# Optimization experiments

Hardware: AMD Instinct MI355X
Metric: run time of the kernel (lower is better)

## Reference

```python
import jax, jax.numpy as jnp
import numpy as np

B, N, D, E, H = 8, 2048, 256, 16, 8
CAP = max(min(N, int(N * 2.0 / E)), 4)  # eval capacity_factor = 2.0 -> 256
EPS = 1e-9
LOSS_COEF = 0.01


def _excl_cumsum(t, axis):
    return jnp.cumsum(t, axis=axis) - t


def _top2_gating(x, w_gating):
    # x: (B, N, D); w_gating: (D, E)
    raw = jax.nn.softmax(jnp.einsum('bnd,de->bne', x, w_gating), axis=-1)
    idx1 = jnp.argmax(raw, axis=-1)
    g1 = jnp.max(raw, axis=-1)
    m1 = jax.nn.one_hot(idx1, E, dtype=raw.dtype)
    gates2 = raw * (1.0 - m1)
    idx2 = jnp.argmax(gates2, axis=-1)
    g2 = jnp.max(gates2, axis=-1)
    m2 = jax.nn.one_hot(idx2, E, dtype=raw.dtype)
    denom = g1 + g2 + EPS
    g1 = g1 / denom
    g2 = g2 / denom
    # load-balance loss
    density_1 = m1.mean(axis=-2)          # (B, E)
    proxy = raw.mean(axis=-2)             # (B, E)
    loss = (proxy * density_1).mean() * float(E * E)
    # second policy == 'all': keep mask_2 as-is
    pos1 = _excl_cumsum(m1, -2) * m1
    m1 = m1 * (pos1 < float(CAP)).astype(m1.dtype)
    m1_count = m1.sum(axis=-2, keepdims=True)
    m1_flat = m1.sum(axis=-1)             # (B, N)
    pos1 = pos1.sum(axis=-1)              # (B, N)
    g1 = g1 * m1_flat
    pos2 = (_excl_cumsum(m2, -2) + m1_count) * m2
    m2 = m2 * (pos2 < float(CAP)).astype(m2.dtype)
    m2_flat = m2.sum(axis=-1)
    pos2 = pos2.sum(axis=-1)
    g2 = g2 * m2_flat
    oh_e1 = jax.nn.one_hot(idx1, E, dtype=raw.dtype)
    oh_e2 = jax.nn.one_hot(idx2, E, dtype=raw.dtype)
    oh_c1 = jax.nn.one_hot(pos1.astype(jnp.int32), CAP, dtype=raw.dtype)
    oh_c2 = jax.nn.one_hot(pos2.astype(jnp.int32), CAP, dtype=raw.dtype)
    # combine: (B, N, E, CAP); note torch applies mask_flat twice (idempotent)
    combine = ((g1 * m1_flat)[..., None, None] * oh_e1[..., :, None] * oh_c1[..., None, :]
               + (g2 * m2_flat)[..., None, None] * oh_e2[..., :, None] * oh_c2[..., None, :])
    dispatch = (combine > 0).astype(combine.dtype)
    return dispatch, combine, loss


def _mixer(xe, audio, Wq, Wkv, Wp, bp):
    # CrossModalMixer, eval mode (dropouts = identity)
    # xe: (B, CAP, D); audio: (B, 1, D)
    b, n, c = xe.shape
    dh = c // H
    scale = dh ** -0.5
    q = (audio @ Wq).reshape(b, 1, H, dh).transpose(0, 2, 1, 3)   # (b,h,1,dh)
    kv = (xe @ Wkv).reshape(b, n, 2, H, dh)
    k = kv[:, :, 0].transpose(0, 2, 1, 3)                          # (b,h,n,dh)
    v = kv[:, :, 1].transpose(0, 2, 1, 3)
    attn = jax.nn.softmax(jnp.einsum('bhqd,bhkd->bhqk', q, k) * scale, axis=-1)
    o = jnp.einsum('bhqk,bhkd->bhqd', attn, v).transpose(0, 2, 1, 3).reshape(b, 1, c)
    gate = jax.nn.sigmoid(o @ Wp + bp)                             # (b,1,c)
    return xe * gate                                               # einsum('bnc,bc->bnc')


def setup_inputs():
    ks = jax.random.split(jax.random.key(0), 7)
    return {
        'x': jax.random.normal(ks[0], (B, N, D), jnp.float32),
        'audio_feat': jax.random.normal(ks[1], (B, 1, D), jnp.float32),
        'w_gating': jax.random.normal(ks[2], (D, E), jnp.float32),
        'Wq': jax.random.normal(ks[3], (E, D, D), jnp.float32) * 0.02,
        'Wkv': jax.random.normal(ks[4], (E, D, 2 * D), jnp.float32) * 0.02,
        'Wp': jax.random.normal(ks[5], (E, D, D), jnp.float32) * 0.02,
        'bp': jnp.zeros((E, D), jnp.float32),
    }


def reference(x, audio_feat, w_gating, Wq, Wkv, Wp, bp):
    dispatch, combine, loss = _top2_gating(x, w_gating)
    expert_in = jnp.einsum('bnd,bnec->ebcd', x, dispatch)          # (E, B, CAP, D)
    outs = jax.vmap(_mixer, in_axes=(0, None, 0, 0, 0, 0))(expert_in, audio_feat, Wq, Wkv, Wp, bp)
    out = jnp.einsum('ebcd,bnec->bnd', outs, combine)
    return out, loss * LOSS_COEF
```

## Files before the change

kernel.cpp:

```cpp
#include <hip/hip_runtime.h>
#include <cstdint>
#include <cstddef>

#define BB 8
#define NN 2048
#define DD 256
#define EE 16
#define HH 8
#define CAPC 256
#define BN (BB*NN)
#define EB (EE*BB)

__global__ __launch_bounds__(256) void fused_gq_kernel(
    const float* __restrict__ x, const float* __restrict__ wg,
    const float* __restrict__ audio, const float* __restrict__ Wq,
    const float* __restrict__ Wkv,
    int* __restrict__ idx1a, int* __restrict__ idx2a,
    float* __restrict__ g1a, float* __restrict__ g2a,
    float* __restrict__ raw_part, float* __restrict__ cnt_part,
    float* __restrict__ rws)
{
  __shared__ union SM {
    struct { float wgS[DD*EE]; float lgp[4][64][17]; } g;
    struct { float aS[DD][8]; float qpart[8][32][9]; float qS[32][8];
             float wkS[DD][33]; } q;
  } sm;
  int tid = threadIdx.x;

  if (blockIdx.x < 256) {
    for (int t = tid; t < DD*EE; t += 256) sm.g.wgS[t] = wg[t];
    __syncthreads();
    int tk = tid & 63, kc = tid >> 6;
    int token0 = blockIdx.x * 64;
    int token = token0 + tk;
    const float4* xr = (const float4*)(x + (size_t)token*DD + kc*64);
    const float4* wg4 = (const float4*)sm.g.wgS;
    float lg[16];
#pragma unroll
    for (int e = 0; e < 16; ++e) lg[e] = 0.f;
#pragma unroll
    for (int d4 = 0; d4 < 16; ++d4) {
      float4 xv = xr[d4];
      float xa[4] = {xv.x, xv.y, xv.z, xv.w};
#pragma unroll
      for (int dd = 0; dd < 4; ++dd) {
        int d = kc*64 + d4*4 + dd;
        float xc = xa[dd];
#pragma unroll
        for (int j = 0; j < 4; ++j) {
          float4 w = wg4[d*4 + j];
          lg[4*j+0] += xc*w.x; lg[4*j+1] += xc*w.y;
          lg[4*j+2] += xc*w.z; lg[4*j+3] += xc*w.w;
        }
      }
    }
#pragma unroll
    for (int e = 0; e < 16; ++e) sm.g.lgp[kc][tk][e] = lg[e];
    __syncthreads();
    if (tid < 64) {
      int lane = tid;
      float l[16];
#pragma unroll
      for (int e = 0; e < 16; ++e)
        l[e] = sm.g.lgp[0][lane][e] + sm.g.lgp[1][lane][e]
             + sm.g.lgp[2][lane][e] + sm.g.lgp[3][lane][e];
      float mx = l[0];
#pragma unroll
      for (int e = 1; e < 16; ++e) mx = fmaxf(mx, l[e]);
      float p[16]; float s = 0.f;
#pragma unroll
      for (int e = 0; e < 16; ++e) { p[e] = expf(l[e] - mx); s += p[e]; }
      int i1 = 0; float b1 = p[0];
#pragma unroll
      for (int e = 1; e < 16; ++e) { if (p[e] > b1) { b1 = p[e]; i1 = e; } }
      float b2 = (i1 == 0) ? 0.f : p[0]; int i2 = 0;
#pragma unroll
      for (int e = 1; e < 16; ++e) { float v = (e == i1) ? 0.f : p[e]; if (v > b2) { b2 = v; i2 = e; } }
      float inv = 1.f / s;
      float g1 = b1*inv, g2 = b2*inv;
      float den = g1 + g2 + 1e-9f;
      g1 /= den; g2 /= den;
      int tok = token0 + lane;
      idx1a[tok] = i1; idx2a[tok] = i2;
      g1a[tok] = g1;   g2a[tok] = g2;
      int blk = blockIdx.x;
#pragma unroll
      for (int e = 0; e < 16; ++e) {
        float v = p[e] * inv;
        v += __shfl_down(v, 32); v += __shfl_down(v, 16);
        v += __shfl_down(v, 8);  v += __shfl_down(v, 4);
        v += __shfl_down(v, 2);  v += __shfl_down(v, 1);
        unsigned long long mb = __ballot(i1 == e);
        if (lane == 0) {
          raw_part[blk*16 + e] = v;
          cnt_part[blk*16 + e] = (float)__popcll(mb);
        }
      }
    }
  } else {
    int eh = blockIdx.x - 256;
    int e = eh >> 3, h = eh & 7;
    for (int i = tid; i < 2048; i += 256) { int b = i >> 8, k = i & 255; sm.q.aS[k][b] = audio[b*DD + k]; }
    __syncthreads();
    int j = tid & 31, kg = tid >> 5;
    const float* wq = Wq + (size_t)e*DD*DD + h*32 + j;
    float acc[8] = {0,0,0,0,0,0,0,0};
#pragma unroll
    for (int i = 0; i < 32; ++i) {
      int k = kg*32 + i;
      float w = wq[(size_t)k*DD];
      float4 a0 = *(const float4*)&sm.q.aS[k][0];
      float4 a1 = *(const float4*)&sm.q.aS[k][4];
      acc[0]+=w*a0.x; acc[1]+=w*a0.y; acc[2]+=w*a0.z; acc[3]+=w*a0.w;
      acc[4]+=w*a1.x; acc[5]+=w*a1.y; acc[6]+=w*a1.z; acc[7]+=w*a1.w;
    }
#pragma unroll
    for (int b = 0; b < 8; ++b) sm.q.qpart[kg][j][b] = acc[b];
    const float* wkbase = Wkv + (size_t)e*(DD*2*DD) + h*32;
    float4 stg[8];
#pragma unroll
    for (int m = 0; m < 8; ++m) {
      int row = m*32 + (tid >> 3), c4 = tid & 7;
      stg[m] = *(const float4*)(wkbase + (size_t)row*(2*DD) + c4*4);
    }
#pragma unroll
    for (int m = 0; m < 8; ++m) {
      int row = m*32 + (tid >> 3), c4 = tid & 7;
      sm.q.wkS[row][c4*4+0] = stg[m].x; sm.q.wkS[row][c4*4+1] = stg[m].y;
      sm.q.wkS[row][c4*4+2] = stg[m].z; sm.q.wkS[row][c4*4+3] = stg[m].w;
    }
    __syncthreads();
    {
      int jj = tid >> 3, b = tid & 7;
      float s = 0.f;
#pragma unroll
      for (int g = 0; g < 8; ++g) s += sm.q.qpart[g][jj][b];
      sm.q.qS[jj][b] = s;
    }
    __syncthreads();
    int d = tid;
    float racc[8] = {0,0,0,0,0,0,0,0};
#pragma unroll
    for (int jj = 0; jj < 32; ++jj) {
      float w = sm.q.wkS[d][jj];
      float4 q0 = *(const float4*)&sm.q.qS[jj][0];
      float4 q1 = *(const float4*)&sm.q.qS[jj][4];
      racc[0]+=w*q0.x; racc[1]+=w*q0.y; racc[2]+=w*q0.z; racc[3]+=w*q0.w;
      racc[4]+=w*q1.x; racc[5]+=w*q1.y; racc[6]+=w*q1.z; racc[7]+=w*q1.w;
    }
#pragma unroll
    for (int b = 0; b < 8; ++b)
      rws[((size_t)(e*8 + b))*2048 + d*8 + h] = racc[b];
  }
}

__global__ __launch_bounds__(256) void scan_kernel(
    const int* __restrict__ idx1a, const int* __restrict__ idx2a,
    float* __restrict__ g1a, float* __restrict__ g2a, int* __restrict__ slot_token,
    const float* __restrict__ raw_part, const float* __restrict__ cnt_part,
    const float* __restrict__ Wkv, const float* __restrict__ Wp,
    float* __restrict__ dummy,
    float* __restrict__ out_loss)
{
  int tid = threadIdx.x;
  if (blockIdx.x >= BB) {
    int pid = (blockIdx.x - BB)*256 + tid;
    const float4* wk4 = (const float4*)Wkv;
    const float4* wp4 = (const float4*)Wp;
    float s = 0.f;
    for (int i = pid; i < 786432; i += 56*256) {
      float4 v = (i < 524288) ? wk4[i] : wp4[i - 524288];
      s += v.x + v.y + v.z + v.w;
    }
    if (s != 0.f) dummy[pid & 1023] = s;
    return;
  }
  __shared__ unsigned long long m1s[16][32], m2s[16][32];
  __shared__ int wp1[16][32], wp2[16][32], mcnt[16];
  int b = blockIdx.x;
  int wave = tid >> 6, lane = tid & 63;
  for (int i = tid; i < 16*CAPC; i += 256) {
    int e = i >> 8, s = i & 255;
    slot_token[(e*BB + b)*CAPC + s] = -1;
  }
  for (int w = wave; w < 32; w += 4) {
    int token = b*NN + w*64 + lane;
    int i1 = idx1a[token], i2 = idx2a[token];
#pragma unroll
    for (int e = 0; e < 16; ++e) {
      unsigned long long ma = __ballot(i1 == e);
      unsigned long long mb = __ballot(i2 == e);
      if (lane == 0) { m1s[e][w] = ma; m2s[e][w] = mb; }
    }
  }
  __syncthreads();
  if (tid < 16) {
    int run = 0;
    for (int w = 0; w < 32; ++w) { wp1[tid][w] = run; run += (int)__popcll(m1s[tid][w]); }
    mcnt[tid] = run < CAPC ? run : CAPC;
  } else if (tid < 32) {
    int e2 = tid - 16; int run = 0;
    for (int w = 0; w < 32; ++w) { wp2[e2][w] = run; run += (int)__popcll(m2s[e2][w]); }
  }
  __syncthreads();
  for (int w = wave; w < 32; w += 4) {
    int token = b*NN + w*64 + lane;
    int i1 = idx1a[token], i2 = idx2a[token];
    unsigned long long lt = (1ull << lane) - 1ull;
    int pos1 = wp1[i1][w] + (int)__popcll(m1s[i1][w] & lt);
    float g1 = g1a[token];
    bool k1 = pos1 < CAPC;
    g1a[token] = k1 ? g1 : 0.f;
    if (k1) slot_token[(i1*BB + b)*CAPC + pos1] = token;
    int pos2 = mcnt[i2] + wp2[i2][w] + (int)__popcll(m2s[i2][w] & lt);
    float g2 = g2a[token];
    bool k2 = pos2 < CAPC;
    g2a[token] = k2 ? g2 : 0.f;
    if (k2 && g2 > 0.f) slot_token[(i2*BB + b)*CAPC + pos2] = token;
  }
  if (blockIdx.x == 0) {
    float v = 0.f;
    if (tid < 128) {
      int bb = tid >> 4, e = tid & 15;
      float rs = 0.f, cs = 0.f;
#pragma unroll 4
      for (int k = 0; k < 32; ++k) {
        rs += raw_part[(bb*32 + k)*16 + e];
        cs += cnt_part[(bb*32 + k)*16 + e];
      }
      v = (rs * (1.f/(float)NN)) * (cs * (1.f/(float)NN));
    }
    v += __shfl_down(v, 32); v += __shfl_down(v, 16); v += __shfl_down(v, 8);
    v += __shfl_down(v, 4);  v += __shfl_down(v, 2);  v += __shfl_down(v, 1);
    __shared__ float r4[4];
    if ((tid & 63) == 0) r4[tid >> 6] = v;
    __syncthreads();
    if (tid == 0)
      out_loss[0] = (r4[0]+r4[1]+r4[2]+r4[3]) * ((float)(EE*EE) / (float)(BB*EE)) * 0.01f;
  }
}

__global__ __launch_bounds__(512) void expert_kernel(
    const float* __restrict__ x, const float* __restrict__ rws,
    const int* __restrict__ slot_token, const float* __restrict__ Wkv,
    const float* __restrict__ Wp, const float* __restrict__ bp,
    float* __restrict__ gateW)
{
  __shared__ float rS[DD][8];
  __shared__ int   tokS[CAPC];
  __shared__ float lp[2][CAPC][9];
  __shared__ float aST[CAPC][8];
  __shared__ float part[2][8][DD];
  __shared__ float xaS[8][DD];
  __shared__ float oS[DD];
  __shared__ float op[2][DD];
  int tid = threadIdx.x;
  int eb = blockIdx.x;
  int e  = eb >> 3;

  {
    const float4* rin = (const float4*)(rws + (size_t)eb*2048);
    ((float4*)rS)[tid] = rin[tid];
    if (tid < CAPC) tokS[tid] = slot_token[eb*CAPC + tid];
  }
  __syncthreads();

  {
    int s = tid >> 1, q = tid & 1;
    int token = tokS[s];
    float l[8] = {0,0,0,0,0,0,0,0};
    if (token >= 0) {
      const float4* xr = (const float4*)(x + (size_t)token*DD) + q;
#pragma unroll
      for (int i = 0; i < 32; ++i) {
        float4 xv = xr[i*2];
        float xa[4] = {xv.x, xv.y, xv.z, xv.w};
#pragma unroll
        for (int dd = 0; dd < 4; ++dd) {
          int d = i*8 + q*4 + dd;
          float4 r0 = *(const float4*)&rS[d][0];
          float4 r1 = *(const float4*)&rS[d][4];
          float xc = xa[dd];
          l[0]+=xc*r0.x; l[1]+=xc*r0.y; l[2]+=xc*r0.z; l[3]+=xc*r0.w;
          l[4]+=xc*r1.x; l[5]+=xc*r1.y; l[6]+=xc*r1.z; l[7]+=xc*r1.w;
        }
      }
    }
#pragma unroll
    for (int h = 0; h < 8; ++h) lp[q][s][h] = l[h];
  }
  __syncthreads();
#pragma unroll
  for (int r = 0; r < 4; ++r) {
    int idx = r*512 + tid;
    int s2 = idx >> 3, h2 = idx & 7;
    aST[s2][h2] = (lp[0][s2][h2] + lp[1][s2][h2]) * 0.17677669529663687f;
  }
  __syncthreads();

  {
    int wave = tid >> 6, lane = tid & 63;
    int h = wave;
    float v0 = aST[lane][h],     v1 = aST[lane+64][h];
    float v2 = aST[lane+128][h], v3 = aST[lane+192][h];
    float m = fmaxf(fmaxf(v0, v1), fmaxf(v2, v3));
    m = fmaxf(m, __shfl_down(m, 32)); m = fmaxf(m, __shfl_down(m, 16));
    m = fmaxf(m, __shfl_down(m, 8));  m = fmaxf(m, __shfl_down(m, 4));
    m = fmaxf(m, __shfl_down(m, 2));  m = fmaxf(m, __shfl_down(m, 1));
    m = __shfl(m, 0);
    float e0 = expf(v0 - m), e1 = expf(v1 - m), e2 = expf(v2 - m), e3 = expf(v3 - m);
    float sm = e0 + e1 + e2 + e3;
    sm += __shfl_down(sm, 32); sm += __shfl_down(sm, 16); sm += __shfl_down(sm, 8);
    sm += __shfl_down(sm, 4);  sm += __shfl_down(sm, 2);  sm += __shfl_down(sm, 1);
    sm = __shfl(sm, 0);
    float inv = 1.f / sm;
    aST[lane][h]     = e0*inv; aST[lane+64][h]  = e1*inv;
    aST[lane+128][h] = e2*inv; aST[lane+192][h] = e3*inv;
  }
  __syncthreads();

  {
    int d = tid & 255, sc = tid >> 8;
    const float* xb = x + d;
    float acc[8] = {0,0,0,0,0,0,0,0};
#pragma unroll 4
    for (int i = 0; i < 128; ++i) {
      int s2 = sc*128 + i;
      int tk = tokS[s2];
      int tkc = tk < 0 ? 0 : tk;
      float msk = tk < 0 ? 0.f : 1.f;
      float xv = xb[(size_t)tkc*DD] * msk;
      float4 a0 = *(const float4*)&aST[s2][0];
      float4 a1 = *(const float4*)&aST[s2][4];
      acc[0]+=a0.x*xv; acc[1]+=a0.y*xv; acc[2]+=a0.z*xv; acc[3]+=a0.w*xv;
      acc[4]+=a1.x*xv; acc[5]+=a1.y*xv; acc[6]+=a1.z*xv; acc[7]+=a1.w*xv;
    }
#pragma unroll
    for (int h = 0; h < 8; ++h) part[sc][h][d] = acc[h];
  }
  __syncthreads();
#pragma unroll
  for (int r = 0; r < 4; ++r) {
    int idx = r*512 + tid;
    int h2 = idx >> 8, d2 = idx & 255;
    xaS[h2][d2] = part[0][h2][d2] + part[1][h2][d2];
  }
  __syncthreads();

  {
    int c = tid & 255, kc = tid >> 8;
    int h = c >> 5;
    const float* wv = Wkv + (size_t)e*(DD*2*DD) + DD + c;
    float a = 0.f;
#pragma unroll 8
    for (int i = 0; i < 128; ++i) {
      int d2 = kc*128 + i;
      a += wv[(size_t)d2*(2*DD)] * xaS[h][d2];
    }
    op[kc][c] = a;
  }
  __syncthreads();
  if (tid < DD) oS[tid] = op[0][tid] + op[1][tid];
  __syncthreads();

  {
    int c = tid & 255, kc = tid >> 8;
    const float* wp = Wp + (size_t)e*DD*DD + c;
    float a = 0.f;
#pragma unroll 8
    for (int i = 0; i < 128; ++i) {
      int d2 = kc*128 + i;
      a += wp[(size_t)d2*DD] * oS[d2];
    }
    op[kc][c] = a;
  }
  __syncthreads();
  if (tid < DD) {
    float sv = bp[e*DD + tid] + op[0][tid] + op[1][tid];
    gateW[(size_t)eb*DD + tid] = 1.f / (1.f + expf(-sv));
  }
}

__global__ __launch_bounds__(256) void out_kernel(
    const float* __restrict__ x, const float* __restrict__ g1f, const float* __restrict__ g2f,
    const int* __restrict__ idx1a, const int* __restrict__ idx2a,
    const float* __restrict__ gateW, float* __restrict__ out)
{
  int idx = blockIdx.x*256 + threadIdx.x;
  int token = idx >> 6;
  int d4 = idx & 63;
  int b = token >> 11;
  float g1 = g1f[token], g2 = g2f[token];
  int e1 = idx1a[token], e2 = idx2a[token];
  float4 w1 = ((const float4*)(gateW + (size_t)(e1*BB+b)*DD))[d4];
  float4 w2 = ((const float4*)(gateW + (size_t)(e2*BB+b)*DD))[d4];
  float4 xv = ((const float4*)x)[idx];
  float4 o;
  o.x = xv.x*(g1*w1.x + g2*w2.x);
  o.y = xv.y*(g1*w1.y + g2*w2.y);
  o.z = xv.z*(g1*w1.z + g2*w2.z);
  o.w = xv.w*(g1*w1.w + g2*w2.w);
  ((float4*)out)[idx] = o;
}

extern "C" void kernel_launch(void* const* d_in, const int* in_sizes, int n_in,
                              void* d_out, int out_size, void* d_ws, size_t ws_size,
                              hipStream_t stream)
{
  const float* x     = (const float*)d_in[0];
  const float* audio = (const float*)d_in[1];
  const float* wg    = (const float*)d_in[2];
  const float* Wq    = (const float*)d_in[3];
  const float* Wkv   = (const float*)d_in[4];
  const float* Wp    = (const float*)d_in[5];
  const float* bp    = (const float*)d_in[6];
  float* out = (float*)d_out;

  float* raw_part = (float*)d_ws;
  float* cnt_part = raw_part + 256*16;
  int*   idx1a   = (int*)(cnt_part + 256*16);
  int*   idx2a   = idx1a + BN;
  float* g1a     = (float*)(idx2a + BN);
  float* g2a     = g1a + BN;
  int*   slot_token = (int*)(g2a + BN);
  float* rws     = (float*)(slot_token + EB*CAPC);
  float* dummy   = rws + (size_t)EB*2048;
  float* gateW   = dummy + 1024;

  fused_gq_kernel<<<384, 256, 0, stream>>>(x, wg, audio, Wq, Wkv,
                                           idx1a, idx2a, g1a, g2a,
                                           raw_part, cnt_part, rws);
  scan_kernel<<<64, 256, 0, stream>>>(idx1a, idx2a, g1a, g2a, slot_token,
                                      raw_part, cnt_part, Wkv, Wp, dummy,
                                      out + (size_t)out_size - 1);
  expert_kernel<<<EB, 512, 0, stream>>>(x, rws, slot_token, Wkv, Wp, bp, gateW);
  out_kernel<<<(BN*DD/4)/256, 256, 0, stream>>>(x, g1a, g2a, idx1a, idx2a, gateW, out);
}
```

Before: 153.3 us.

## Fold capacity scan into expert kernel and drop scan launch

Removes the separate scan kernel. Each expert block now computes its own per-(expert,batch) capacity positions with ballots over idx arrays, builds the slot→token map in shared memory and zeroes dropped gates. The load-balance loss reduction moves to the last block of the output kernel, and the L2 prefetch blocks move into the gating kernel, now reading only the V half of Wkv plus Wp. This saves one launch and the slot_token global round trip, but each of the 128 expert blocks redundantly scans 2048 indices.

New measurement: 140.4 us. -8.4%, faster.

```diff
diff --git a/kernel.cpp b/kernel.cpp
--- a/kernel.cpp
+++ b/kernel.cpp
@@ -14,11 +14,11 @@
 __global__ __launch_bounds__(256) void fused_gq_kernel(
     const float* __restrict__ x, const float* __restrict__ wg,
     const float* __restrict__ audio, const float* __restrict__ Wq,
-    const float* __restrict__ Wkv,
+    const float* __restrict__ Wkv, const float* __restrict__ Wp,
     int* __restrict__ idx1a, int* __restrict__ idx2a,
     float* __restrict__ g1a, float* __restrict__ g2a,
     float* __restrict__ raw_part, float* __restrict__ cnt_part,
-    float* __restrict__ rws)
+    float* __restrict__ rws, float* __restrict__ dummy)
 {
   __shared__ union SM {
     struct { float wgS[DD*EE]; float lgp[4][64][17]; } g;
@@ -26,6 +26,26 @@
              float wkS[DD][33]; } q;
   } sm;
   int tid = threadIdx.x;
+
+  if (blockIdx.x >= 384) {
+    int pid = (blockIdx.x - 384)*256 + tid;
+    const float4* wk4 = (const float4*)Wkv;
+    const float4* wp4 = (const float4*)Wp;
+    float s = 0.f;
+    for (int i = pid; i < 524288; i += 64*256) {
+      float4 v;
+      if (i < 262144) {
+        int e = i >> 14, rem = i & 16383;
+        int row = rem >> 6, c4 = rem & 63;
+        v = wk4[e*32768 + row*128 + 64 + c4];
+      } else {
+        v = wp4[i - 262144];
+      }
+      s += v.x + v.y + v.z + v.w;
+    }
+    if (s != 0.f) dummy[pid & 1023] = s;
+    return;
+  }
 
   if (blockIdx.x < 256) {
     for (int t = tid; t < DD*EE; t += 256) sm.g.wgS[t] = wg[t];
@@ -154,95 +174,11 @@
   }
 }
 
-__global__ __launch_bounds__(256) void scan_kernel(
-    const int* __restrict__ idx1a, const int* __restrict__ idx2a,
-    float* __restrict__ g1a, float* __restrict__ g2a, int* __restrict__ slot_token,
-    const float* __restrict__ raw_part, const float* __restrict__ cnt_part,
-    const float* __restrict__ Wkv, const float* __restrict__ Wp,
-    float* __restrict__ dummy,
-    float* __restrict__ out_loss)
-{
-  int tid = threadIdx.x;
-  if (blockIdx.x >= BB) {
-    int pid = (blockIdx.x - BB)*256 + tid;
-    const float4* wk4 = (const float4*)Wkv;
-    const float4* wp4 = (const float4*)Wp;
-    float s = 0.f;
-    for (int i = pid; i < 786432; i += 56*256) {
-      float4 v = (i < 524288) ? wk4[i] : wp4[i - 524288];
-      s += v.x + v.y + v.z + v.w;
-    }
-    if (s != 0.f) dummy[pid & 1023] = s;
-    return;
-  }
-  __shared__ unsigned long long m1s[16][32], m2s[16][32];
-  __shared__ int wp1[16][32], wp2[16][32], mcnt[16];
-  int b = blockIdx.x;
-  int wave = tid >> 6, lane = tid & 63;
-  for (int i = tid; i < 16*CAPC; i += 256) {
-    int e = i >> 8, s = i & 255;
-    slot_token[(e*BB + b)*CAPC + s] = -1;
-  }
-  for (int w = wave; w < 32; w += 4) {
-    int token = b*NN + w*64 + lane;
-    int i1 = idx1a[token], i2 = idx2a[token];
-#pragma unroll
-    for (int e = 0; e < 16; ++e) {
-      unsigned long long ma = __ballot(i1 == e);
-      unsigned long long mb = __ballot(i2 == e);
-      if (lane == 0) { m1s[e][w] = ma; m2s[e][w] = mb; }
-    }
-  }
-  __syncthreads();
-  if (tid < 16) {
-    int run = 0;
-    for (int w = 0; w < 32; ++w) { wp1[tid][w] = run; run += (int)__popcll(m1s[tid][w]); }
-    mcnt[tid] = run < CAPC ? run : CAPC;
-  } else if (tid < 32) {
-    int e2 = tid - 16; int run = 0;
-    for (int w = 0; w < 32; ++w) { wp2[e2][w] = run; run += (int)__popcll(m2s[e2][w]); }
-  }
-  __syncthreads();
-  for (int w = wave; w < 32; w += 4) {
-    int token = b*NN + w*64 + lane;
-    int i1 = idx1a[token], i2 = idx2a[token];
-    unsigned long long lt = (1ull << lane) - 1ull;
-    int pos1 = wp1[i1][w] + (int)__popcll(m1s[i1][w] & lt);
-    float g1 = g1a[token];
-    bool k1 = pos1 < CAPC;
-    g1a[token] = k1 ? g1 : 0.f;
-    if (k1) slot_token[(i1*BB + b)*CAPC + pos1] = token;
-    int pos2 = mcnt[i2] + wp2[i2][w] + (int)__popcll(m2s[i2][w] & lt);
-    float g2 = g2a[token];
-    bool k2 = pos2 < CAPC;
-    g2a[token] = k2 ? g2 : 0.f;
-    if (k2 && g2 > 0.f) slot_token[(i2*BB + b)*CAPC + pos2] = token;
-  }
-  if (blockIdx.x == 0) {
-    float v = 0.f;
-    if (tid < 128) {
-      int bb = tid >> 4, e = tid & 15;
-      float rs = 0.f, cs = 0.f;
-#pragma unroll 4
-      for (int k = 0; k < 32; ++k) {
-        rs += raw_part[(bb*32 + k)*16 + e];
-        cs += cnt_part[(bb*32 + k)*16 + e];
-      }
-      v = (rs * (1.f/(float)NN)) * (cs * (1.f/(float)NN));
-    }
-    v += __shfl_down(v, 32); v += __shfl_down(v, 16); v += __shfl_down(v, 8);
-    v += __shfl_down(v, 4);  v += __shfl_down(v, 2);  v += __shfl_down(v, 1);
-    __shared__ float r4[4];
-    if ((tid & 63) == 0) r4[tid >> 6] = v;
-    __syncthreads();
-    if (tid == 0)
-      out_loss[0] = (r4[0]+r4[1]+r4[2]+r4[3]) * ((float)(EE*EE) / (float)(BB*EE)) * 0.01f;
-  }
-}
-
 __global__ __launch_bounds__(512) void expert_kernel(
     const float* __restrict__ x, const float* __restrict__ rws,
-    const int* __restrict__ slot_token, const float* __restrict__ Wkv,
+    const int* __restrict__ idx1a, const int* __restrict__ idx2a,
+    float* __restrict__ g1a, float* __restrict__ g2a,
+    const float* __restrict__ Wkv,
     const float* __restrict__ Wp, const float* __restrict__ bp,
     float* __restrict__ gateW)
 {
@@ -254,14 +190,60 @@
   __shared__ float xaS[8][DD];
   __shared__ float oS[DD];
   __shared__ float op[2][DD];
+  __shared__ unsigned long long s_m1[32], s_m2[32];
+  __shared__ int s_wp1[32], s_wp2[32], s_m1cnt;
   int tid = threadIdx.x;
   int eb = blockIdx.x;
   int e  = eb >> 3;
+  int b  = eb & 7;
 
   {
     const float4* rin = (const float4*)(rws + (size_t)eb*2048);
     ((float4*)rS)[tid] = rin[tid];
-    if (tid < CAPC) tokS[tid] = slot_token[eb*CAPC + tid];
+    if (tid < CAPC) tokS[tid] = -1;
+  }
+  int wave = tid >> 6, lane = tid & 63;
+  {
+#pragma unroll
+    for (int cc = 0; cc < 4; ++cc) {
+      int c = wave*4 + cc;
+      int token = b*NN + c*64 + lane;
+      int i1 = idx1a[token], i2 = idx2a[token];
+      unsigned long long ma = __ballot(i1 == e);
+      unsigned long long mb = __ballot(i2 == e);
+      if (lane == 0) { s_m1[c] = ma; s_m2[c] = mb; }
+    }
+  }
+  __syncthreads();
+  if (tid == 0) {
+    int run = 0;
+    for (int c = 0; c < 32; ++c) { s_wp1[c] = run; run += (int)__popcll(s_m1[c]); }
+    s_m1cnt = run < CAPC ? run : CAPC;
+  } else if (tid == 64) {
+    int run = 0;
+    for (int c = 0; c < 32; ++c) { s_wp2[c] = run; run += (int)__popcll(s_m2[c]); }
+  }
+  __syncthreads();
+  {
+    int m1cnt = s_m1cnt;
+#pragma unroll
+    for (int cc = 0; cc < 4; ++cc) {
+      int c = wave*4 + cc;
+      int token = b*NN + c*64 + lane;
+      int i1 = idx1a[token], i2 = idx2a[token];
+      unsigned long long lt = (1ull << lane) - 1ull;
+      if (i1 == e) {
+        int pos1 = s_wp1[c] + (int)__popcll(s_m1[c] & lt);
+        if (pos1 < CAPC) tokS[pos1] = token;
+        else g1a[token] = 0.f;
+      }
+      if (i2 == e) {
+        int pos2 = m1cnt + s_wp2[c] + (int)__popcll(s_m2[c] & lt);
+        if (pos2 < CAPC) {
+          if (g2a[token] > 0.f) tokS[pos2] = token;
+        } else g2a[token] = 0.f;
+      }
+    }
   }
   __syncthreads();
 
@@ -299,7 +281,6 @@
   __syncthreads();
 
   {
-    int wave = tid >> 6, lane = tid & 63;
     int h = wave;
     float v0 = aST[lane][h],     v1 = aST[lane+64][h];
     float v2 = aST[lane+128][h], v3 = aST[lane+192][h];
@@ -384,7 +365,9 @@
 __global__ __launch_bounds__(256) void out_kernel(
     const float* __restrict__ x, const float* __restrict__ g1f, const float* __restrict__ g2f,
     const int* __restrict__ idx1a, const int* __restrict__ idx2a,
-    const float* __restrict__ gateW, float* __restrict__ out)
+    const float* __restrict__ gateW,
+    const float* __restrict__ raw_part, const float* __restrict__ cnt_part,
+    float* __restrict__ out, float* __restrict__ out_loss)
 {
   int idx = blockIdx.x*256 + threadIdx.x;
   int token = idx >> 6;
@@ -401,6 +384,28 @@
   o.z = xv.z*(g1*w1.z + g2*w2.z);
   o.w = xv.w*(g1*w1.w + g2*w2.w);
   ((float4*)out)[idx] = o;
+
+  if (blockIdx.x == gridDim.x - 1) {
+    int tid = threadIdx.x;
+    float v = 0.f;
+    if (tid < 128) {
+      int bb = tid >> 4, e = tid & 15;
+      float rs = 0.f, cs = 0.f;
+#pragma unroll 4
+      for (int k = 0; k < 32; ++k) {
+        rs += raw_part[(bb*32 + k)*16 + e];
+        cs += cnt_part[(bb*32 + k)*16 + e];
+      }
+      v = (rs * (1.f/(float)NN)) * (cs * (1.f/(float)NN));
+    }
+    v += __shfl_down(v, 32); v += __shfl_down(v, 16); v += __shfl_down(v, 8);
+    v += __shfl_down(v, 4);  v += __shfl_down(v, 2);  v += __shfl_down(v, 1);
+    __shared__ float r4[4];
+    if ((tid & 63) == 0) r4[tid >> 6] = v;
+    __syncthreads();
+    if (tid == 0)
+      out_loss[0] = (r4[0]+r4[1]+r4[2]+r4[3]) * ((float)(EE*EE) / (float)(BB*EE)) * 0.01f;
+  }
 }
 
 extern "C" void kernel_launch(void* const* d_in, const int* in_sizes, int n_in,
@@ -422,17 +427,16 @@
   int*   idx2a   = idx1a + BN;
   float* g1a     = (float*)(idx2a + BN);
   float* g2a     = g1a + BN;
-  int*   slot_token = (int*)(g2a + BN);
-  float* rws     = (float*)(slot_token + EB*CAPC);
+  float* rws     = g2a + BN;
   float* dummy   = rws + (size_t)EB*2048;
   float* gateW   = dummy + 1024;
 
-  fused_gq_kernel<<<384, 256, 0, stream>>>(x, wg, audio, Wq, Wkv,
+  fused_gq_kernel<<<448, 256, 0, stream>>>(x, wg, audio, Wq, Wkv, Wp,
                                            idx1a, idx2a, g1a, g2a,
-                                           raw_part, cnt_part, rws);
-  scan_kernel<<<64, 256, 0, stream>>>(idx1a, idx2a, g1a, g2a, slot_token,
-                                      raw_part, cnt_part, Wkv, Wp, dummy,
-                                      out + (size_t)out_size - 1);
-  expert_kernel<<<EB, 512, 0, stream>>>(x, rws, slot_token, Wkv, Wp, bp, gateW);
-  out_kernel<<<(BN*DD/4)/256, 256, 0, stream>>>(x, g1a, g2a, idx1a, idx2a, gateW, out);
+                                           raw_part, cnt_part, rws, dummy);
+  expert_kernel<<<EB, 512, 0, stream>>>(x, rws, idx1a, idx2a, g1a, g2a,
+                                        Wkv, Wp, bp, gateW);
+  out_kernel<<<(BN*DD/4)/256, 256, 0, stream>>>(x, g1a, g2a, idx1a, idx2a, gateW,
+                                                raw_part, cnt_part,
+                                                out, out + (size_t)out_size - 1);
 }
```
